# Optimization experiments

Measured on AMD Instinct MI355X. Metric: run time of the kernel, lower is better.

The kernel has to match this reference:

```python
import jax, jax.numpy as jnp
import numpy as np


def setup_inputs() -> dict:
    key = jax.random.key(0)
    k1, k2, k3, k4 = jax.random.split(key, 4)
    B, S, E = 2, 2048, 2048
    scale = 0.02  # keep logits in a sane range
    return {
        "x": jax.random.normal(k1, (B, S, E), dtype=jnp.float32),
        "rotation_params": jax.random.normal(k2, (E, E), dtype=jnp.float32) * scale,
        "entangle_params": jax.random.normal(k3, (E, E), dtype=jnp.float32) * scale,
        "w_out": jax.random.normal(k4, (E, E), dtype=jnp.float32) * scale,
        "num_heads": 16,
    }


def reference(x, rotation_params, entangle_params, w_out, num_heads):
    # x: (B, S, E); rotation/entangle/w_out: (E, E)
    B, S, E = x.shape
    H = num_heads
    hd = E // H
    q = x @ rotation_params.T          # (B, S, E)
    k = x @ entangle_params.T          # (B, S, E)
    v = x                              # identity V projection, per source
    qh = q.reshape(B, S, H, hd)
    kh = k.reshape(B, S, H, hd)
    vh = v.reshape(B, S, H, hd)
    scores = jnp.einsum("bqhd,bkhd->bhqk", qh, kh) / np.sqrt(hd)
    # per-head bias branch from source; statically dead when E != H but kept faithful
    if entangle_params.shape[0] == H:
        scores = scores + entangle_params.reshape(H, 1, 1)
    attn = jax.nn.softmax(scores, axis=-1)  # dropout is identity at inference
    out = jnp.einsum("bhqk,bkhd->bqhd", attn, vh).reshape(B, S, E)
    return out @ w_out.T
```

## Files before the change

kernel.cpp:

```cpp
#include <hip/hip_runtime.h>

typedef __attribute__((ext_vector_type(8))) __bf16 bf16x8;
typedef __attribute__((ext_vector_type(4))) float f32x4;
typedef unsigned short u16;
typedef unsigned int u32;

__device__ __forceinline__ u16 f2bf_bits(float f) {
  union { float f; u32 u; } v; v.f = f;
  u32 r = (v.u + 0x7fffu + ((v.u >> 16) & 1u)) >> 16;
  return (u16)r;
}

__device__ __forceinline__ void gload_lds16(const u16* g, u16* l) {
  __builtin_amdgcn_global_load_lds(
      (const __attribute__((address_space(1))) void*)g,
      (__attribute__((address_space(3))) void*)l, 16, 0, 0);
}

__device__ __forceinline__ bf16x8 lds_read8(const u16* base, int byteoff) {
  return *reinterpret_cast<const bf16x8*>(reinterpret_cast<const char*>(base) + byteoff);
}

__global__ void cast_bf16_kernel(const float* __restrict__ in, u16* __restrict__ out, int n4) {
  int i = blockIdx.x * blockDim.x + threadIdx.x;
  if (i >= n4) return;
  float4 v = reinterpret_cast<const float4*>(in)[i];
  ushort4 o;
  o.x = f2bf_bits(v.x); o.y = f2bf_bits(v.y);
  o.z = f2bf_bits(v.z); o.w = f2bf_bits(v.w);
  reinterpret_cast<ushort4*>(out)[i] = o;
}

__global__ void build_vt_kernel(const float* __restrict__ x, u16* __restrict__ vt, int S, int E, int H) {
  __shared__ float t[32][33];
  const int bh = blockIdx.z, b = bh / H, h = bh % H;
  const int s0 = blockIdx.x * 32, d0 = blockIdx.y * 32;
  const int tx = threadIdx.x & 31, ty = threadIdx.x >> 5;
  const float* xp = x + ((size_t)b * S) * E + (size_t)h * 128;
  #pragma unroll
  for (int r = ty; r < 32; r += 8)
    t[r][tx] = xp[(size_t)(s0 + r) * E + d0 + tx];
  __syncthreads();
  u16* vp = vt + ((size_t)bh * 128 + d0) * S + s0;
  #pragma unroll
  for (int r = ty; r < 32; r += 8)
    vp[(size_t)r * S + tx] = f2bf_bits(t[tx][r]);
}

template <bool BF16OUT>
__global__ __launch_bounds__(512) void gemm2_kernel(const u16* __restrict__ A,
                                                    const u16* __restrict__ B0,
                                                    const u16* __restrict__ B1,
                                                    void* __restrict__ C0,
                                                    void* __restrict__ C1,
                                                    int M, int N, int K) {
  __shared__ __align__(16) u16 As[3][128 * 64];
  __shared__ __align__(16) u16 Bs[3][256 * 64];
  const u16* Bt = blockIdx.z ? B1 : B0;
  void* Cout = blockIdx.z ? C1 : C0;
  const int tid = threadIdx.x;
  const int wave = tid >> 6, lane = tid & 63;
  const int lr = lane & 15, lh = lane >> 4;
  const int nbn = N >> 8;
  const int nwg = gridDim.x;
  const int bid = blockIdx.x;
  const int wg = (bid & 7) * (nwg >> 3) + (bid >> 3);
  const int bm = wg / nbn, bn = wg % nbn;
  const int m0 = bm << 7, n0 = bn << 8;
  const int wr = wave >> 2, wc = wave & 3;

  const f32x4 zf = {0.f, 0.f, 0.f, 0.f};
  f32x4 acc[4][4];
  #pragma unroll
  for (int i = 0; i < 4; ++i)
    #pragma unroll
    for (int j = 0; j < 4; ++j) acc[i][j] = zf;

  const u16* agp[2]; int adst[2];
  const u16* bgp[4]; int bdst[4];
  #pragma unroll
  for (int i = 0; i < 2; ++i) {
    const int db = i * 8192 + tid * 16;
    const int row = db >> 7;
    const int cb = (db & 127) ^ ((row & 7) << 4);
    agp[i] = A + (size_t)(m0 + row) * K + (cb >> 1);
    adst[i] = (i * 8192 + wave * 1024) >> 1;
  }
  #pragma unroll
  for (int i = 0; i < 4; ++i) {
    const int db = i * 8192 + tid * 16;
    const int row = db >> 7;
    const int cb = (db & 127) ^ ((row & 7) << 4);
    bgp[i] = Bt + (size_t)(n0 + row) * K + (cb >> 1);
    bdst[i] = (i * 8192 + wave * 1024) >> 1;
  }

  const int NT = K >> 6;

  #pragma unroll
  for (int i = 0; i < 2; ++i) gload_lds16(agp[i], &As[0][adst[i]]);
  #pragma unroll
  for (int i = 0; i < 4; ++i) gload_lds16(bgp[i], &Bs[0][bdst[i]]);
  #pragma unroll
  for (int i = 0; i < 2; ++i) gload_lds16(agp[i] + 64, &As[1][adst[i]]);
  #pragma unroll
  for (int i = 0; i < 4; ++i) gload_lds16(bgp[i] + 64, &Bs[1][bdst[i]]);
  asm volatile("s_waitcnt vmcnt(6)" ::: "memory");
  __builtin_amdgcn_sched_barrier(0);
  __builtin_amdgcn_s_barrier();

  for (int t = 0; t < NT; ++t) {
    const int cur = t % 3;
    if (t + 2 < NT) {
      const int sb = (t + 2) % 3;
      const int k0 = (t + 2) << 6;
      #pragma unroll
      for (int i = 0; i < 2; ++i) gload_lds16(agp[i] + k0, &As[sb][adst[i]]);
      #pragma unroll
      for (int i = 0; i < 4; ++i) gload_lds16(bgp[i] + k0, &Bs[sb][bdst[i]]);
    }
    bf16x8 af[4][2], bfv[4][2];
    #pragma unroll
    for (int i = 0; i < 4; ++i) {
      #pragma unroll
      for (int s = 0; s < 2; ++s) {
        const int rowA = wr * 64 + i * 16 + lr;
        af[i][s] = lds_read8(As[cur], rowA * 128 + ((s * 64 + lh * 16) ^ ((rowA & 7) << 4)));
        const int rowB = wc * 64 + i * 16 + lr;
        bfv[i][s] = lds_read8(Bs[cur], rowB * 128 + ((s * 64 + lh * 16) ^ ((rowB & 7) << 4)));
      }
    }
    __builtin_amdgcn_s_setprio(1);
    #pragma unroll
    for (int s = 0; s < 2; ++s)
      #pragma unroll
      for (int i = 0; i < 4; ++i)
        #pragma unroll
        for (int j = 0; j < 4; ++j)
          acc[i][j] = __builtin_amdgcn_mfma_f32_16x16x32_bf16(af[i][s], bfv[j][s], acc[i][j], 0, 0, 0);
    __builtin_amdgcn_s_setprio(0);
    asm volatile("s_waitcnt lgkmcnt(0)" ::: "memory");
    if (t + 2 < NT) {
      asm volatile("s_waitcnt vmcnt(6)" ::: "memory");
    } else {
      asm volatile("s_waitcnt vmcnt(0)" ::: "memory");
    }
    __builtin_amdgcn_sched_barrier(0);
    __builtin_amdgcn_s_barrier();
  }

  #pragma unroll
  for (int i = 0; i < 4; ++i) {
    const int row0 = m0 + wr * 64 + i * 16 + lh * 4;
    #pragma unroll
    for (int j = 0; j < 4; ++j) {
      const int col = n0 + wc * 64 + j * 16 + lr;
      #pragma unroll
      for (int r = 0; r < 4; ++r) {
        const size_t idx = (size_t)(row0 + r) * N + col;
        if (BF16OUT)
          ((u16*)Cout)[idx] = f2bf_bits(acc[i][j][r]);
        else
          ((float*)Cout)[idx] = acc[i][j][r];
      }
    }
  }
}

__global__ __launch_bounds__(256, 4) void attn_kernel(const u16* __restrict__ Q,
                                                      const u16* __restrict__ Kx,
                                                      const u16* __restrict__ Vt,
                                                      u16* __restrict__ O,
                                                      int S, int E, int H) {
  __shared__ __align__(16) u16 Ks[64 * 128];
  __shared__ __align__(16) u16 Vs[128 * 64];
  __shared__ __align__(16) u16 Pl[4][16 * 64];

  const int tid = threadIdx.x;
  const int wave = tid >> 6, lane = tid & 63;
  const int lr = lane & 15, lh = lane >> 4;
  const int qb = blockIdx.x;
  const int bh = blockIdx.y;
  const int b = bh / H, h = bh % H;
  const size_t base = ((size_t)b * S) * E + (size_t)h * 128;
  const u16* Qp = Q + base;
  const u16* Kp = Kx + base;
  const u16* Vp = Vt + (size_t)bh * 128 * S;
  u16* Op = O + base;

  const int qrow = qb * 64 + wave * 16 + lr;
  bf16x8 qf[4];
  #pragma unroll
  for (int c = 0; c < 4; ++c)
    qf[c] = *reinterpret_cast<const bf16x8*>(Qp + (size_t)qrow * E + c * 32 + lh * 8);

  const int dstb = wave * 1024 + lane * 16;
  int ksrc[4], vsrc[4];
  u16 *kdst[4], *vdst[4];
  #pragma unroll
  for (int i = 0; i < 4; ++i) {
    const int db = dstb + i * 4096;
    const int s = db >> 8;
    const int kcb = (db & 255) ^ ((s & 7) << 4);
    ksrc[i] = s * E + (kcb >> 1);
    kdst[i] = Ks + ((wave * 1024 + i * 4096) >> 1);
    const int d = db >> 7;
    const int vcb = (db & 127) ^ ((d & 7) << 4);
    vsrc[i] = d * S + (vcb >> 1);
    vdst[i] = Vs + ((wave * 1024 + i * 4096) >> 1);
  }

  const f32x4 zf = {0.f, 0.f, 0.f, 0.f};
  f32x4 oacc[8];
  #pragma unroll
  for (int n = 0; n < 8; ++n) oacc[n] = zf;
  float Lp[4] = {0.f, 0.f, 0.f, 0.f};

  const float c2 = 0.12751649736230842f;
  const int swz = (lr & 7) << 4;
  u16* pw = &Pl[wave][0];

  for (int s0 = 0; s0 < S; s0 += 64) {
    #pragma unroll
    for (int i = 0; i < 4; ++i) gload_lds16(Kp + s0 * E + ksrc[i], kdst[i]);
    #pragma unroll
    for (int i = 0; i < 4; ++i) gload_lds16(Vp + s0 + vsrc[i], vdst[i]);
    __syncthreads();

    f32x4 sg[4];
    #pragma unroll
    for (int g = 0; g < 4; ++g) sg[g] = zf;
    #pragma unroll
    for (int c = 0; c < 4; ++c) {
      const int cb = (c * 64 + lh * 16) ^ swz;
      #pragma unroll
      for (int g = 0; g < 4; ++g) {
        bf16x8 kf = lds_read8(Ks, (g * 16 + lr) * 256 + cb);
        sg[g] = __builtin_amdgcn_mfma_f32_16x16x32_bf16(qf[c], kf, sg[g], 0, 0, 0);
      }
    }

    float p[4][4];
    #pragma unroll
    for (int g = 0; g < 4; ++g)
      #pragma unroll
      for (int j = 0; j < 4; ++j)
        p[g][j] = __builtin_exp2f(sg[g][j] * c2);
    #pragma unroll
    for (int j = 0; j < 4; ++j)
      Lp[j] += (p[0][j] + p[1][j]) + (p[2][j] + p[3][j]);

    #pragma unroll
    for (int j = 0; j < 4; ++j) {
      const int r = lh * 4 + j;
      const int rx = (r & 7) << 4;
      #pragma unroll
      for (int g = 0; g < 4; ++g) {
        const int cbp = ((g * 16 + lr) * 2) ^ rx;
        *reinterpret_cast<u16*>(reinterpret_cast<char*>(pw) + r * 128 + cbp) = f2bf_bits(p[g][j]);
      }
    }

    #pragma unroll
    for (int ks = 0; ks < 2; ++ks) {
      const int cb = ks * 64 + lh * 16;
      bf16x8 pf = lds_read8(pw, lr * 128 + (cb ^ swz));
      #pragma unroll
      for (int n = 0; n < 8; ++n) {
        bf16x8 vf = lds_read8(Vs, (n * 16 + lr) * 128 + (cb ^ swz));
        oacc[n] = __builtin_amdgcn_mfma_f32_16x16x32_bf16(pf, vf, oacc[n], 0, 0, 0);
      }
    }
    __syncthreads();
  }

  #pragma unroll
  for (int m = 1; m <= 8; m <<= 1)
    #pragma unroll
    for (int j = 0; j < 4; ++j)
      Lp[j] += __shfl_xor(Lp[j], m, 64);

  float inv[4];
  #pragma unroll
  for (int j = 0; j < 4; ++j) inv[j] = 1.0f / Lp[j];
  const int orow0 = qb * 64 + wave * 16 + lh * 4;
  #pragma unroll
  for (int n = 0; n < 8; ++n)
    #pragma unroll
    for (int j = 0; j < 4; ++j)
      Op[(size_t)(orow0 + j) * E + n * 16 + lr] = f2bf_bits(oacc[n][j] * inv[j]);
}

extern "C" void kernel_launch(void* const* d_in, const int* in_sizes, int n_in,
                              void* d_out, int out_size, void* d_ws, size_t ws_size,
                              hipStream_t stream) {
  const float* x    = (const float*)d_in[0];
  const float* rot  = (const float*)d_in[1];
  const float* ent  = (const float*)d_in[2];
  const float* wout = (const float*)d_in[3];
  const int B = 2, S = 2048, E = 2048, H = 16;
  const int M = B * S;
  const size_t nBSE = (size_t)M * E;
  const size_t nEE = (size_t)E * E;

  u16* xb = (u16*)d_ws;
  u16* qb = xb + nBSE;
  u16* kb = qb + nBSE;
  u16* rb = (u16*)d_out;
  u16* eb = rb + nEE;
  u16* vt = eb + nEE;
  u16* wb = kb;
  u16* ob = xb;

  cast_bf16_kernel<<<(int)(nBSE / 4 / 256), 256, 0, stream>>>(x, xb, (int)(nBSE / 4));
  cast_bf16_kernel<<<(int)(nEE / 4 / 256), 256, 0, stream>>>(rot, rb, (int)(nEE / 4));
  cast_bf16_kernel<<<(int)(nEE / 4 / 256), 256, 0, stream>>>(ent, eb, (int)(nEE / 4));

  dim3 tg(S / 32, 128 / 32, B * H);
  build_vt_kernel<<<tg, 256, 0, stream>>>(x, vt, S, E, H);

  const int g2 = (M / 128) * (E / 256);
  gemm2_kernel<true><<<dim3(g2, 1, 2), 512, 0, stream>>>(xb, rb, eb, qb, kb, M, E, E);

  dim3 ag(S / 64, B * H);
  attn_kernel<<<ag, 256, 0, stream>>>(qb, kb, vt, ob, S, E, H);

  cast_bf16_kernel<<<(int)(nEE / 4 / 256), 256, 0, stream>>>(wout, wb, (int)(nEE / 4));

  gemm2_kernel<false><<<dim3(g2, 1, 1), 512, 0, stream>>>(ob, wb, wb, d_out, d_out, M, E, E);
}
```

Before: 383.0 us.

## Enlarge GEMM tiles to 256x256 with double buffering and XCD-aware block mapping

Replaces the 128x256 triple-buffered GEMM with a 256x256-tile, double-buffered kernel. Each wave now computes 128x64, reusing each B fragment across eight A row-blocks to cut LDS traffic per MFMA. A hardcoded mapping sends the Q/K projections (z=0/1) and tile coordinates to specific XCDs for L2 locality. The change also switches bf16 conversion to the native cast and raises wave priority around the attention MFMAs. Risks: fewer workgroups (128 for the output GEMM) may underfill the 256 CUs, the grid mapping is hardcoded for 4096x2048, and two-stage buffering plus a full __syncthreads per k-step hides less latency.

New measurement: 375.9 us. Within noise of the previous version (-1.8%).

```diff
diff --git a/kernel.cpp b/kernel.cpp
--- a/kernel.cpp
+++ b/kernel.cpp
@@ -6,9 +6,10 @@
 typedef unsigned int u32;
 
 __device__ __forceinline__ u16 f2bf_bits(float f) {
-  union { float f; u32 u; } v; v.f = f;
-  u32 r = (v.u + 0x7fffu + ((v.u >> 16) & 1u)) >> 16;
-  return (u16)r;
+  __bf16 h = (__bf16)f;
+  u16 r;
+  __builtin_memcpy(&r, &h, 2);
+  return r;
 }
 
 __device__ __forceinline__ void gload_lds16(const u16* g, u16* l) {
@@ -48,110 +49,92 @@
 }
 
 template <bool BF16OUT>
-__global__ __launch_bounds__(512) void gemm2_kernel(const u16* __restrict__ A,
-                                                    const u16* __restrict__ B0,
-                                                    const u16* __restrict__ B1,
-                                                    void* __restrict__ C0,
-                                                    void* __restrict__ C1,
-                                                    int M, int N, int K) {
-  __shared__ __align__(16) u16 As[3][128 * 64];
-  __shared__ __align__(16) u16 Bs[3][256 * 64];
-  const u16* Bt = blockIdx.z ? B1 : B0;
-  void* Cout = blockIdx.z ? C1 : C0;
+__global__ __launch_bounds__(512, 2) void gemm3_kernel(const u16* __restrict__ A,
+                                                       const u16* __restrict__ B0,
+                                                       const u16* __restrict__ B1,
+                                                       void* __restrict__ C0,
+                                                       void* __restrict__ C1,
+                                                       int K, int N, int zmask) {
+  __shared__ __align__(16) u16 As[2][256 * 64];
+  __shared__ __align__(16) u16 Bs[2][256 * 64];
   const int tid = threadIdx.x;
   const int wave = tid >> 6, lane = tid & 63;
   const int lr = lane & 15, lh = lane >> 4;
-  const int nbn = N >> 8;
-  const int nwg = gridDim.x;
   const int bid = blockIdx.x;
-  const int wg = (bid & 7) * (nwg >> 3) + (bid >> 3);
-  const int bm = wg / nbn, bn = wg % nbn;
-  const int m0 = bm << 7, n0 = bn << 8;
+  const int xcd = bid & 7;
+  const int slot = bid >> 3;
+  const int z = slot & zmask;
+  const int c = zmask ? (slot >> 1) : slot;
+  const int bm = (xcd >> 1) * 4 + (c >> 2);
+  const int bn = (xcd & 1) * 4 + (c & 3);
+  const int m0 = bm << 8, n0 = bn << 8;
+  const u16* Bt = z ? B1 : B0;
+  void* Cout = z ? C1 : C0;
   const int wr = wave >> 2, wc = wave & 3;
 
   const f32x4 zf = {0.f, 0.f, 0.f, 0.f};
-  f32x4 acc[4][4];
-  #pragma unroll
-  for (int i = 0; i < 4; ++i)
+  f32x4 acc[8][4];
+  #pragma unroll
+  for (int i = 0; i < 8; ++i)
     #pragma unroll
     for (int j = 0; j < 4; ++j) acc[i][j] = zf;
 
-  const u16* agp[2]; int adst[2];
-  const u16* bgp[4]; int bdst[4];
-  #pragma unroll
-  for (int i = 0; i < 2; ++i) {
+  const u16* agp[4]; const u16* bgp[4]; int ldst[4];
+  #pragma unroll
+  for (int i = 0; i < 4; ++i) {
     const int db = i * 8192 + tid * 16;
     const int row = db >> 7;
     const int cb = (db & 127) ^ ((row & 7) << 4);
     agp[i] = A + (size_t)(m0 + row) * K + (cb >> 1);
-    adst[i] = (i * 8192 + wave * 1024) >> 1;
-  }
-  #pragma unroll
-  for (int i = 0; i < 4; ++i) {
-    const int db = i * 8192 + tid * 16;
-    const int row = db >> 7;
-    const int cb = (db & 127) ^ ((row & 7) << 4);
     bgp[i] = Bt + (size_t)(n0 + row) * K + (cb >> 1);
-    bdst[i] = (i * 8192 + wave * 1024) >> 1;
+    ldst[i] = (i * 8192 + wave * 1024) >> 1;
   }
 
   const int NT = K >> 6;
 
   #pragma unroll
-  for (int i = 0; i < 2; ++i) gload_lds16(agp[i], &As[0][adst[i]]);
-  #pragma unroll
-  for (int i = 0; i < 4; ++i) gload_lds16(bgp[i], &Bs[0][bdst[i]]);
-  #pragma unroll
-  for (int i = 0; i < 2; ++i) gload_lds16(agp[i] + 64, &As[1][adst[i]]);
-  #pragma unroll
-  for (int i = 0; i < 4; ++i) gload_lds16(bgp[i] + 64, &Bs[1][bdst[i]]);
-  asm volatile("s_waitcnt vmcnt(6)" ::: "memory");
-  __builtin_amdgcn_sched_barrier(0);
-  __builtin_amdgcn_s_barrier();
-
+  for (int i = 0; i < 4; ++i) gload_lds16(agp[i], &As[0][ldst[i]]);
+  #pragma unroll
+  for (int i = 0; i < 4; ++i) gload_lds16(bgp[i], &Bs[0][ldst[i]]);
+  __syncthreads();
+
+  int cur = 0;
   for (int t = 0; t < NT; ++t) {
-    const int cur = t % 3;
-    if (t + 2 < NT) {
-      const int sb = (t + 2) % 3;
-      const int k0 = (t + 2) << 6;
-      #pragma unroll
-      for (int i = 0; i < 2; ++i) gload_lds16(agp[i] + k0, &As[sb][adst[i]]);
-      #pragma unroll
-      for (int i = 0; i < 4; ++i) gload_lds16(bgp[i] + k0, &Bs[sb][bdst[i]]);
-    }
-    bf16x8 af[4][2], bfv[4][2];
-    #pragma unroll
-    for (int i = 0; i < 4; ++i) {
-      #pragma unroll
-      for (int s = 0; s < 2; ++s) {
-        const int rowA = wr * 64 + i * 16 + lr;
-        af[i][s] = lds_read8(As[cur], rowA * 128 + ((s * 64 + lh * 16) ^ ((rowA & 7) << 4)));
-        const int rowB = wc * 64 + i * 16 + lr;
-        bfv[i][s] = lds_read8(Bs[cur], rowB * 128 + ((s * 64 + lh * 16) ^ ((rowB & 7) << 4)));
-      }
+    if (t + 1 < NT) {
+      const int k0 = (t + 1) << 6;
+      #pragma unroll
+      for (int i = 0; i < 4; ++i) gload_lds16(agp[i] + k0, &As[cur ^ 1][ldst[i]]);
+      #pragma unroll
+      for (int i = 0; i < 4; ++i) gload_lds16(bgp[i] + k0, &Bs[cur ^ 1][ldst[i]]);
+    }
+    bf16x8 bfr[4][2];
+    #pragma unroll
+    for (int j = 0; j < 4; ++j) {
+      const int rowB = wc * 64 + j * 16 + lr;
+      #pragma unroll
+      for (int ks = 0; ks < 2; ++ks)
+        bfr[j][ks] = lds_read8(Bs[cur], rowB * 128 + ((ks * 64 + lh * 16) ^ ((rowB & 7) << 4)));
     }
     __builtin_amdgcn_s_setprio(1);
     #pragma unroll
-    for (int s = 0; s < 2; ++s)
-      #pragma unroll
-      for (int i = 0; i < 4; ++i)
-        #pragma unroll
-        for (int j = 0; j < 4; ++j)
-          acc[i][j] = __builtin_amdgcn_mfma_f32_16x16x32_bf16(af[i][s], bfv[j][s], acc[i][j], 0, 0, 0);
+    for (int i = 0; i < 8; ++i) {
+      const int rowA = wr * 128 + i * 16 + lr;
+      bf16x8 af0 = lds_read8(As[cur], rowA * 128 + ((lh * 16) ^ ((rowA & 7) << 4)));
+      bf16x8 af1 = lds_read8(As[cur], rowA * 128 + ((64 + lh * 16) ^ ((rowA & 7) << 4)));
+      #pragma unroll
+      for (int j = 0; j < 4; ++j) {
+        acc[i][j] = __builtin_amdgcn_mfma_f32_16x16x32_bf16(af0, bfr[j][0], acc[i][j], 0, 0, 0);
+        acc[i][j] = __builtin_amdgcn_mfma_f32_16x16x32_bf16(af1, bfr[j][1], acc[i][j], 0, 0, 0);
+      }
+    }
     __builtin_amdgcn_s_setprio(0);
-    asm volatile("s_waitcnt lgkmcnt(0)" ::: "memory");
-    if (t + 2 < NT) {
-      asm volatile("s_waitcnt vmcnt(6)" ::: "memory");
-    } else {
-      asm volatile("s_waitcnt vmcnt(0)" ::: "memory");
-    }
-    __builtin_amdgcn_sched_barrier(0);
-    __builtin_amdgcn_s_barrier();
-  }
-
-  #pragma unroll
-  for (int i = 0; i < 4; ++i) {
-    const int row0 = m0 + wr * 64 + i * 16 + lh * 4;
+    __syncthreads();
+    cur ^= 1;
+  }
+
+  #pragma unroll
+  for (int i = 0; i < 8; ++i) {
+    const int row0 = m0 + wr * 128 + i * 16 + lh * 4;
     #pragma unroll
     for (int j = 0; j < 4; ++j) {
       const int col = n0 + wc * 64 + j * 16 + lr;
@@ -230,6 +213,7 @@
     f32x4 sg[4];
     #pragma unroll
     for (int g = 0; g < 4; ++g) sg[g] = zf;
+    __builtin_amdgcn_s_setprio(1);
     #pragma unroll
     for (int c = 0; c < 4; ++c) {
       const int cb = (c * 64 + lh * 16) ^ swz;
@@ -239,6 +223,7 @@
         sg[g] = __builtin_amdgcn_mfma_f32_16x16x32_bf16(qf[c], kf, sg[g], 0, 0, 0);
       }
     }
+    __builtin_amdgcn_s_setprio(0);
 
     float p[4][4];
     #pragma unroll
@@ -265,11 +250,13 @@
     for (int ks = 0; ks < 2; ++ks) {
       const int cb = ks * 64 + lh * 16;
       bf16x8 pf = lds_read8(pw, lr * 128 + (cb ^ swz));
+      __builtin_amdgcn_s_setprio(1);
       #pragma unroll
       for (int n = 0; n < 8; ++n) {
         bf16x8 vf = lds_read8(Vs, (n * 16 + lr) * 128 + (cb ^ swz));
         oacc[n] = __builtin_amdgcn_mfma_f32_16x16x32_bf16(pf, vf, oacc[n], 0, 0, 0);
       }
+      __builtin_amdgcn_s_setprio(0);
     }
     __syncthreads();
   }
@@ -319,13 +306,12 @@
   dim3 tg(S / 32, 128 / 32, B * H);
   build_vt_kernel<<<tg, 256, 0, stream>>>(x, vt, S, E, H);
 
-  const int g2 = (M / 128) * (E / 256);
-  gemm2_kernel<true><<<dim3(g2, 1, 2), 512, 0, stream>>>(xb, rb, eb, qb, kb, M, E, E);
+  gemm3_kernel<true><<<256, 512, 0, stream>>>(xb, rb, eb, qb, kb, E, E, 1);
 
   dim3 ag(S / 64, B * H);
   attn_kernel<<<ag, 256, 0, stream>>>(qb, kb, vt, ob, S, E, H);
 
   cast_bf16_kernel<<<(int)(nEE / 4 / 256), 256, 0, stream>>>(wout, wb, (int)(nEE / 4));
 
-  gemm2_kernel<false><<<dim3(g2, 1, 1), 512, 0, stream>>>(ob, wb, wb, d_out, d_out, M, E, E);
-}
+  gemm3_kernel<false><<<128, 512, 0, stream>>>(ob, wb, wb, d_out, d_out, E, E, 0);
+}
```
